# Performance work log

Measured on AMD Instinct MI355X. Metric: run time of the kernel, lower is better.

## Reference

```python
import jax, jax.numpy as jnp
import numpy as np

E = 7          # ensemble_size
STATE = 32
ACTION = 8
HID = [256, 256, 256, 128]
B = 32768


def _init_linear(key, e, fan_in, fan_out):
    kw, kb = jax.random.split(key)
    bound = 1.0 / np.sqrt(fan_in)
    W = jax.random.uniform(kw, (e, fan_in, fan_out), jnp.float32, -bound, bound)
    b = jax.random.uniform(kb, (e, fan_out), jnp.float32, -bound, bound)
    return W, b


def setup_inputs() -> dict:
    key = jax.random.key(0)
    ks = jax.random.split(key, 9)
    state = jax.random.normal(ks[0], (B, STATE), jnp.float32)
    action = jax.random.normal(ks[1], (B, ACTION), jnp.float32)
    dims = [STATE + ACTION] + HID
    W0, b0 = _init_linear(ks[2], E, dims[0], dims[1])
    W1, b1 = _init_linear(ks[3], E, dims[1], dims[2])
    W2, b2 = _init_linear(ks[4], E, dims[2], dims[3])
    W3, b3 = _init_linear(ks[5], E, dims[3], dims[4])
    Wmu, bmu = _init_linear(ks[6], E, dims[4], STATE)
    Wsig, bsig = _init_linear(ks[7], E, dims[4], STATE)
    max_logstd = jnp.ones((STATE,), jnp.float32)
    min_logstd = jnp.full((STATE,), -5.0, jnp.float32)
    return {
        'state': state, 'action': action,
        'W0': W0, 'b0': b0, 'W1': W1, 'b1': b1,
        'W2': W2, 'b2': b2, 'W3': W3, 'b3': b3,
        'Wmu': Wmu, 'bmu': bmu, 'Wsig': Wsig, 'bsig': bsig,
        'max_logstd': max_logstd, 'min_logstd': min_logstd,
    }


def _swish(x):
    return x * jax.nn.sigmoid(x)


def _soft_clamp(x, _min, _max):
    x = _max - jax.nn.softplus(_max - x)
    x = _min + jax.nn.softplus(x - _min)
    return x


def reference(state, action, W0, b0, W1, b1, W2, b2, W3, b3,
              Wmu, bmu, Wsig, bsig, max_logstd, min_logstd):
    # Broadcast inputs to the ensemble axis: [E, B, D]
    x = jnp.concatenate([state, action], axis=-1)            # [B, S+A]
    h = jnp.broadcast_to(x, (E,) + x.shape)                   # [E, B, S+A]
    # Batched per-ensemble GEMM chain (grouped GEMM)
    h = _swish(jnp.einsum('ebi,eio->ebo', h, W0) + b0[:, None, :])
    h = _swish(jnp.einsum('ebi,eio->ebo', h, W1) + b1[:, None, :])
    h = _swish(jnp.einsum('ebi,eio->ebo', h, W2) + b2[:, None, :])
    h = _swish(jnp.einsum('ebi,eio->ebo', h, W3) + b3[:, None, :])
    mu = jnp.einsum('ebi,eio->ebo', h, Wmu) + bmu[:, None, :]         # [E, B, S]
    log_sigma = jnp.einsum('ebi,eio->ebo', h, Wsig) + bsig[:, None, :]
    log_sigma = _soft_clamp(log_sigma, min_logstd, max_logstd)
    sigma = jnp.exp(log_sigma)
    mu = mu + state[None, :, :]                                        # residual
    return mu, sigma
```

## Files before the change

### kernel.cpp

```cpp
#include <hip/hip_runtime.h>
#include <hip/hip_bf16.h>


#define NE 7
#define NB 32768
#define PER_E 188416
#define HSTRIDE 264

typedef __attribute__((ext_vector_type(8))) short short8;
typedef __attribute__((ext_vector_type(4))) float floatx4;

__device__ __forceinline__ short f2b(float f) {
    union { float f; unsigned u; } c; c.f = f;
    return (short)((c.u + 0x7fffu + ((c.u >> 16) & 1u)) >> 16);
}
__device__ __forceinline__ unsigned pk2(float a, float b) {
    union { __hip_bfloat162 h; unsigned u; } c;
    c.h = __float22bfloat162_rn(make_float2(a, b));
    return c.u;
}

__global__ void __launch_bounds__(256) pack_w(
    const float* __restrict__ W0, const float* __restrict__ W1,
    const float* __restrict__ W2, const float* __restrict__ W3,
    const float* __restrict__ Wmu, const float* __restrict__ Wsig,
    short* __restrict__ out)
{
    __shared__ float tile[32][65];
    const int t = threadIdx.x;
    int b = blockIdx.x;
    int e = b / 92;
    int r = b - e * 92;
    const float* src = W0;
    int off = 0, Kact = 40, N = 256, NT = 16, kt, ntb;
    bool inv = false, head = false;
    if (r < 8)       { kt = r >> 2; ntb = r & 3; }
    else if (r < 40) { r -= 8;  src = W1; off = 16384;  Kact = 256; kt = r >> 2; ntb = r & 3; inv = true; }
    else if (r < 72) { r -= 40; src = W2; off = 81920;  Kact = 256; kt = r >> 2; ntb = r & 3; inv = true; }
    else if (r < 88) { r -= 72; src = W3; off = 147456; Kact = 256; N = 128; NT = 8; kt = r >> 1; ntb = r & 1; inv = true; }
    else             { r -= 88; off = 180224; Kact = 128; N = 64; NT = 4; kt = r; ntb = 0; inv = true; head = true; }

#pragma unroll
    for (int i = 0; i < 8; ++i) {
        int elem  = t + i * 256;
        int row_l = elem >> 6, col_l = elem & 63;
        int gk = kt * 32 + row_l;
        int gn = ntb * 64 + col_l;
        float v = 0.f;
        if (gk < Kact) {
            if (head) v = (gn < 32) ? Wmu[((size_t)e * 128 + gk) * 32 + gn]
                                    : Wsig[((size_t)e * 128 + gk) * 32 + (gn - 32)];
            else      v = src[((size_t)e * Kact + gk) * N + gn];
        }
        tile[row_l][col_l] = v;
    }
    __syncthreads();

    const int f = t >> 6, lam = t & 63;
    const int lan = lam & 15, quad = lam >> 4;
    short8 o;
#pragma unroll
    for (int j = 0; j < 8; ++j) {
        int q  = quad * 8 + j;
        int sr = inv ? (((q & 1) << 4) | (q >> 1)) : q;
        o[j] = f2b(tile[sr][f * 16 + lan]);
    }
    *(short8*)(out + (size_t)e * PER_E + off +
               ((size_t)(kt * NT + ntb * 4 + f) * 64 + lam) * 8) = o;
}

template<int KT, int NTW, int NT, int NNTW>
__device__ __forceinline__ void mlp_layer(const short* __restrict__ wpk,
                                          const float* __restrict__ bias,
                                          short* hs, const int wave, const int lane,
                                          const short8* bf0,
                                          const short* __restrict__ nwpk,
                                          short8* nbf0) {
    const int quad = lane >> 4;
    const int lan  = lane & 15;
    floatx4 acc[4][NTW];
#pragma unroll
    for (int mt = 0; mt < 4; ++mt)
#pragma unroll
        for (int nt = 0; nt < NTW; ++nt) acc[mt][nt] = floatx4{0.f, 0.f, 0.f, 0.f};

    short8 bfc[NTW], bfn[NTW];
#pragma unroll
    for (int nt = 0; nt < NTW; ++nt) bfc[nt] = bf0[nt];

#pragma unroll
    for (int kt = 0; kt < KT; ++kt) {
        if (kt + 1 < KT) {
#pragma unroll
            for (int nt = 0; nt < NTW; ++nt)
                bfn[nt] = *(const short8*)(wpk +
                    ((size_t)((kt + 1) * NT + wave * NTW + nt) * 64 + lane) * 8);
        }
        short8 af[4];
#pragma unroll
        for (int mt = 0; mt < 4; ++mt)
            af[mt] = *(const short8*)(hs + (mt * 16 + lan) * HSTRIDE + kt * 32 + quad * 8);
#pragma unroll
        for (int nt = 0; nt < NTW; ++nt)
#pragma unroll
            for (int mt = 0; mt < 4; ++mt)
                acc[mt][nt] = __builtin_amdgcn_mfma_f32_16x16x32_bf16(af[mt], bfc[nt], acc[mt][nt], 0, 0, 0);
#pragma unroll
        for (int nt = 0; nt < NTW; ++nt) bfc[nt] = bfn[nt];
    }

#pragma unroll
    for (int nt = 0; nt < NNTW; ++nt)
        nbf0[nt] = *(const short8*)(nwpk + ((size_t)(wave * NNTW + nt) * 64 + lane) * 8);

    __syncthreads();
#pragma unroll
    for (int np = 0; np < NTW / 2; ++np) {
        const int ntg   = wave * NTW + 2 * np;
        const float bA  = bias[ntg * 16 + lan];
        const float bB  = bias[ntg * 16 + 16 + lan];
        const int pcol  = (ntg >> 1) * 32 + 2 * lan;
#pragma unroll
        for (int mt = 0; mt < 4; ++mt)
#pragma unroll
            for (int r2 = 0; r2 < 4; ++r2) {
                float vA = acc[mt][2 * np][r2] + bA;
                vA = vA * __builtin_amdgcn_rcpf(1.f + __expf(-vA));
                float vB = acc[mt][2 * np + 1][r2] + bB;
                vB = vB * __builtin_amdgcn_rcpf(1.f + __expf(-vB));
                *(unsigned*)(hs + (mt * 16 + quad * 4 + r2) * HSTRIDE + pcol) = pk2(vA, vB);
            }
    }
    __syncthreads();
}

__device__ __forceinline__ float softplus_stable(float x) {
    return fmaxf(x, 0.f) + __logf(1.f + __expf(-fabsf(x)));
}

__global__ void __launch_bounds__(256, 3)
fused_ensemble(const float* __restrict__ state, const float* __restrict__ action,
               const float* __restrict__ b0, const float* __restrict__ b1,
               const float* __restrict__ b2, const float* __restrict__ b3,
               const float* __restrict__ bmu, const float* __restrict__ bsig,
               const float* __restrict__ maxls, const float* __restrict__ minls,
               const short* __restrict__ wpk,
               float* __restrict__ out_mu, float* __restrict__ out_sig) {
    __shared__ __align__(16) short hs[64 * HSTRIDE];
    const int tid  = threadIdx.x;
    const int wave = tid >> 6, lane = tid & 63;
    const int bid  = blockIdx.x;
    const int e    = bid >> 9;
    const int r0   = (bid & 511) << 6;

    const short* wp = wpk + (size_t)e * PER_E;

    short8 fragA[4], fragB[4];
#pragma unroll
    for (int nt = 0; nt < 4; ++nt)
        fragA[nt] = *(const short8*)(wp + ((size_t)(wave * 4 + nt) * 64 + lane) * 8);

    for (int idx = tid; idx < 64 * 32; idx += 256) {
        int m = idx >> 5, cp = idx & 31;
        int row = r0 + m;
        float2 v;
        if (cp < 16)      v = ((const float2*)state)[row * 16 + cp];
        else if (cp < 20) v = ((const float2*)action)[row * 4 + (cp - 16)];
        else              v = make_float2(0.f, 0.f);
        *(unsigned*)(hs + m * HSTRIDE + 2 * cp) = pk2(v.x, v.y);
    }
    __syncthreads();

    mlp_layer<2, 4, 16, 4>(wp,          b0 + e * 256, hs, wave, lane, fragA, wp + 16384,  fragB);
    mlp_layer<8, 4, 16, 4>(wp + 16384,  b1 + e * 256, hs, wave, lane, fragB, wp + 81920,  fragA);
    mlp_layer<8, 4, 16, 2>(wp + 81920,  b2 + e * 256, hs, wave, lane, fragA, wp + 147456, fragB);
    mlp_layer<8, 2, 8, 1 >(wp + 147456, b3 + e * 128, hs, wave, lane, fragB, wp + 180224, fragA);

    const int quad = lane >> 4, lan = lane & 15;
    floatx4 acc[4];
#pragma unroll
    for (int mt = 0; mt < 4; ++mt) acc[mt] = floatx4{0.f, 0.f, 0.f, 0.f};
    const short* wph = wp + 180224;
    short8 bhc = fragA[0], bhn;
#pragma unroll
    for (int kt = 0; kt < 4; ++kt) {
        if (kt < 3)
            bhn = *(const short8*)(wph + (((size_t)(kt + 1) * 4 + wave) * 64 + lane) * 8);
#pragma unroll
        for (int mt = 0; mt < 4; ++mt) {
            const short8 af = *(const short8*)(hs + (mt * 16 + lan) * HSTRIDE + kt * 32 + quad * 8);
            acc[mt] = __builtin_amdgcn_mfma_f32_16x16x32_bf16(af, bhc, acc[mt], 0, 0, 0);
        }
        bhc = bhn;
    }
    const int colw = wave * 16 + lan;
    if (colw < 32) {
        const int col = colw;
        const float bv = bmu[e * 32 + col];
#pragma unroll
        for (int mt = 0; mt < 4; ++mt)
#pragma unroll
            for (int r2 = 0; r2 < 4; ++r2) {
                int grow = r0 + mt * 16 + quad * 4 + r2;
                float v = acc[mt][r2] + bv + state[grow * 32 + col];
                out_mu[((size_t)e * NB + grow) * 32 + col] = v;
            }
    } else {
        const int col = colw - 32;
        const float bv = bsig[e * 32 + col];
        const float mx = maxls[col], mn = minls[col];
#pragma unroll
        for (int mt = 0; mt < 4; ++mt)
#pragma unroll
            for (int r2 = 0; r2 < 4; ++r2) {
                int grow = r0 + mt * 16 + quad * 4 + r2;
                float ls = acc[mt][r2] + bv;
                ls = mx - softplus_stable(mx - ls);
                ls = mn + softplus_stable(ls - mn);
                out_sig[((size_t)e * NB + grow) * 32 + col] = __expf(ls);
            }
    }
}

extern "C" void kernel_launch(void* const* d_in, const int* in_sizes, int n_in,
                              void* d_out, int out_size, void* d_ws, size_t ws_size,
                              hipStream_t stream) {
    const float* state  = (const float*)d_in[0];
    const float* action = (const float*)d_in[1];
    const float* W0   = (const float*)d_in[2];
    const float* b0   = (const float*)d_in[3];
    const float* W1   = (const float*)d_in[4];
    const float* b1   = (const float*)d_in[5];
    const float* W2   = (const float*)d_in[6];
    const float* b2   = (const float*)d_in[7];
    const float* W3   = (const float*)d_in[8];
    const float* b3   = (const float*)d_in[9];
    const float* Wmu  = (const float*)d_in[10];
    const float* bmu  = (const float*)d_in[11];
    const float* Wsig = (const float*)d_in[12];
    const float* bsig = (const float*)d_in[13];
    const float* maxls = (const float*)d_in[14];
    const float* minls = (const float*)d_in[15];

    short* wpk = (short*)d_ws;
    float* out_mu  = (float*)d_out;
    float* out_sig = out_mu + (size_t)NE * NB * 32;

    pack_w<<<NE * 92, 256, 0, stream>>>(W0, W1, W2, W3, Wmu, Wsig, wpk);
    fused_ensemble<<<NE * 512, 256, 0, stream>>>(state, action, b0, b1, b2, b3,
                                                 bmu, bsig, maxls, minls, wpk,
                                                 out_mu, out_sig);
}
```

Before: 227.3 us.

## Overlap each layer's swish epilogue with the next layer's MFMA K-loop

Restructures the MLP chain so the epilogue of one layer (bias, swish, bf16 writeback to LDS) is interleaved with the MFMA accumulation of the next layer. The K-tiles of the next layer are reordered: even K-tiles run first while the second half of the previous epilogue is written, and odd K-tiles run after a barrier. This hides the transcendental/ALU epilogue under matrix-core work, but keeps two accumulator sets live at once, which raises VGPR pressure and may hurt occupancy under the 3-blocks-per-SM launch bound.

```diff
diff --git a/kernel.cpp b/kernel.cpp
--- a/kernel.cpp
+++ b/kernel.cpp
@@ -69,67 +69,90 @@
                ((size_t)(kt * NT + ntb * 4 + f) * 64 + lam) * 8) = o;
 }
 
-template<int KT, int NTW, int NT, int NNTW>
-__device__ __forceinline__ void mlp_layer(const short* __restrict__ wpk,
-                                          const float* __restrict__ bias,
-                                          short* hs, const int wave, const int lane,
-                                          const short8* bf0,
-                                          const short* __restrict__ nwpk,
-                                          short8* nbf0) {
-    const int quad = lane >> 4;
-    const int lan  = lane & 15;
-    floatx4 acc[4][NTW];
-#pragma unroll
-    for (int mt = 0; mt < 4; ++mt)
-#pragma unroll
-        for (int nt = 0; nt < NTW; ++nt) acc[mt][nt] = floatx4{0.f, 0.f, 0.f, 0.f};
-
-    short8 bfc[NTW], bfn[NTW];
-#pragma unroll
-    for (int nt = 0; nt < NTW; ++nt) bfc[nt] = bf0[nt];
-
-#pragma unroll
-    for (int kt = 0; kt < KT; ++kt) {
-        if (kt + 1 < KT) {
-#pragma unroll
-            for (int nt = 0; nt < NTW; ++nt)
-                bfn[nt] = *(const short8*)(wpk +
-                    ((size_t)((kt + 1) * NT + wave * NTW + nt) * 64 + lane) * 8);
-        }
-        short8 af[4];
-#pragma unroll
-        for (int mt = 0; mt < 4; ++mt)
-            af[mt] = *(const short8*)(hs + (mt * 16 + lan) * HSTRIDE + kt * 32 + quad * 8);
-#pragma unroll
-        for (int nt = 0; nt < NTW; ++nt)
-#pragma unroll
-            for (int mt = 0; mt < 4; ++mt)
-                acc[mt][nt] = __builtin_amdgcn_mfma_f32_16x16x32_bf16(af[mt], bfc[nt], acc[mt][nt], 0, 0, 0);
-#pragma unroll
-        for (int nt = 0; nt < NTW; ++nt) bfc[nt] = bfn[nt];
-    }
-
-#pragma unroll
-    for (int nt = 0; nt < NNTW; ++nt)
-        nbf0[nt] = *(const short8*)(nwpk + ((size_t)(wave * NNTW + nt) * 64 + lane) * 8);
-
-    __syncthreads();
-#pragma unroll
-    for (int np = 0; np < NTW / 2; ++np) {
-        const int ntg   = wave * NTW + 2 * np;
-        const float bA  = bias[ntg * 16 + lan];
-        const float bB  = bias[ntg * 16 + 16 + lan];
-        const int pcol  = (ntg >> 1) * 32 + 2 * lan;
-#pragma unroll
-        for (int mt = 0; mt < 4; ++mt)
-#pragma unroll
-            for (int r2 = 0; r2 < 4; ++r2) {
-                float vA = acc[mt][2 * np][r2] + bA;
-                vA = vA * __builtin_amdgcn_rcpf(1.f + __expf(-vA));
-                float vB = acc[mt][2 * np + 1][r2] + bB;
-                vB = vB * __builtin_amdgcn_rcpf(1.f + __expf(-vB));
-                *(unsigned*)(hs + (mt * 16 + quad * 4 + r2) * HSTRIDE + pcol) = pk2(vA, vB);
-            }
+
+template<int NTW, int NT>
+__device__ __forceinline__ void ldb(const short* __restrict__ wpk, int kt,
+                                    int wave, int lane, short8* bf) {
+#pragma unroll
+    for (int nt = 0; nt < NTW; ++nt)
+        bf[nt] = *(const short8*)(wpk + ((size_t)(kt * NT + wave * NTW + nt) * 64 + lane) * 8);
+}
+
+template<int NTW>
+__device__ __forceinline__ void mfma_k(floatx4 (&acc)[4][NTW], const short* hs,
+                                       int kt, int lan, int quad, const short8* bfc) {
+    short8 af[4];
+#pragma unroll
+    for (int mt = 0; mt < 4; ++mt)
+        af[mt] = *(const short8*)(hs + (mt * 16 + lan) * HSTRIDE + kt * 32 + quad * 8);
+#pragma unroll
+    for (int nt = 0; nt < NTW; ++nt)
+#pragma unroll
+        for (int mt = 0; mt < 4; ++mt)
+            acc[mt][nt] = __builtin_amdgcn_mfma_f32_16x16x32_bf16(af[mt], bfc[nt], acc[mt][nt], 0, 0, 0);
+}
+
+__device__ __forceinline__ float swish(float v) {
+    return v * __builtin_amdgcn_rcpf(1.f + __expf(-v));
+}
+
+template<int NTW>
+__device__ __forceinline__ void epi_q(const floatx4 (&acc)[4][NTW], int np, int mt,
+                                      float bA, float bB, short* hs,
+                                      int wave, int lan, int quad) {
+    const int ntg  = wave * NTW + 2 * np;
+    const int pcol = (ntg >> 1) * 32 + 2 * lan;
+#pragma unroll
+    for (int r2 = 0; r2 < 4; ++r2) {
+        float vA = swish(acc[mt][2 * np][r2] + bA);
+        float vB = swish(acc[mt][2 * np + 1][r2] + bB);
+        *(unsigned*)(hs + (mt * 16 + quad * 4 + r2) * HSTRIDE + pcol) = pk2(vA, vB);
+    }
+}
+
+template<int NNTW, int NNT, int XNTW, int XNT>
+__device__ __forceinline__ void layer_step(
+    const short* __restrict__ wpkN, const short* __restrict__ wpkX,
+    const float* __restrict__ biasP,
+    floatx4 (&accP)[4][4], floatx4 (&accN)[4][NNTW],
+    short8 (&bfN)[NNTW], short8 (&bfX)[XNTW],
+    short* hs, int wave, int lane, int lan, int quad)
+{
+    const int ntg0 = wave * 4;
+    const float bA0 = biasP[ntg0 * 16 + lan],       bB0 = biasP[ntg0 * 16 + 16 + lan];
+    const float bA1 = biasP[(ntg0 + 2) * 16 + lan], bB1 = biasP[(ntg0 + 2) * 16 + 16 + lan];
+
+#pragma unroll
+    for (int mt = 0; mt < 4; ++mt)
+        epi_q<4>(accP, 0, mt, bA0, bB0, hs, wave, lan, quad);
+    __syncthreads();
+
+#pragma unroll
+    for (int mt = 0; mt < 4; ++mt)
+#pragma unroll
+        for (int nt = 0; nt < NNTW; ++nt) accN[mt][nt] = floatx4{0.f, 0.f, 0.f, 0.f};
+
+    short8 bfc[NNTW], bfn[NNTW];
+#pragma unroll
+    for (int nt = 0; nt < NNTW; ++nt) bfc[nt] = bfN[nt];
+
+#pragma unroll
+    for (int i = 0; i < 4; ++i) {
+        ldb<NNTW, NNT>(wpkN, (i < 3) ? 2 * i + 2 : 1, wave, lane, bfn);
+        mfma_k<NNTW>(accN, hs, 2 * i, lan, quad, bfc);
+        epi_q<4>(accP, 1, i, bA1, bB1, hs, wave, lan, quad);
+#pragma unroll
+        for (int nt = 0; nt < NNTW; ++nt) bfc[nt] = bfn[nt];
+    }
+    __syncthreads();
+
+#pragma unroll
+    for (int i = 0; i < 4; ++i) {
+        if (i < 3) ldb<NNTW, NNT>(wpkN, 2 * i + 3, wave, lane, bfn);
+        else       ldb<XNTW, XNT>(wpkX, 0, wave, lane, bfX);
+        mfma_k<NNTW>(accN, hs, 2 * i + 1, lan, quad, bfc);
+#pragma unroll
+        for (int nt = 0; nt < NNTW; ++nt) bfc[nt] = bfn[nt];
     }
     __syncthreads();
 }
@@ -149,16 +172,15 @@
     __shared__ __align__(16) short hs[64 * HSTRIDE];
     const int tid  = threadIdx.x;
     const int wave = tid >> 6, lane = tid & 63;
+    const int lan  = lane & 15, quad = lane >> 4;
     const int bid  = blockIdx.x;
     const int e    = bid >> 9;
     const int r0   = (bid & 511) << 6;
 
     const short* wp = wpk + (size_t)e * PER_E;
 
-    short8 fragA[4], fragB[4];
-#pragma unroll
-    for (int nt = 0; nt < 4; ++nt)
-        fragA[nt] = *(const short8*)(wp + ((size_t)(wave * 4 + nt) * 64 + lane) * 8);
+    short8 bfL0[4], bfL0b[4], bfL1[4], bfL2[4], bfL3[2], bfHD[1];
+    ldb<4, 16>(wp, 0, wave, lane, bfL0);
 
     for (int idx = tid; idx < 64 * 32; idx += 256) {
         int m = idx >> 5, cp = idx & 31;
@@ -171,17 +193,40 @@
     }
     __syncthreads();
 
-    mlp_layer<2, 4, 16, 4>(wp,          b0 + e * 256, hs, wave, lane, fragA, wp + 16384,  fragB);
-    mlp_layer<8, 4, 16, 4>(wp + 16384,  b1 + e * 256, hs, wave, lane, fragB, wp + 81920,  fragA);
-    mlp_layer<8, 4, 16, 2>(wp + 81920,  b2 + e * 256, hs, wave, lane, fragA, wp + 147456, fragB);
-    mlp_layer<8, 2, 8, 1 >(wp + 147456, b3 + e * 128, hs, wave, lane, fragB, wp + 180224, fragA);
-
-    const int quad = lane >> 4, lan = lane & 15;
+    floatx4 acc0[4][4], acc1[4][4], acc2[4][4];
+    floatx4 acc3[4][2];
+#pragma unroll
+    for (int mt = 0; mt < 4; ++mt)
+#pragma unroll
+        for (int nt = 0; nt < 4; ++nt) acc0[mt][nt] = floatx4{0.f, 0.f, 0.f, 0.f};
+    ldb<4, 16>(wp, 1, wave, lane, bfL0b);
+    mfma_k<4>(acc0, hs, 0, lan, quad, bfL0);
+    ldb<4, 16>(wp + 16384, 0, wave, lane, bfL1);
+    mfma_k<4>(acc0, hs, 1, lan, quad, bfL0b);
+    __syncthreads();
+
+    layer_step<4, 16, 4, 16>(wp + 16384,  wp + 81920,  b0 + e * 256,
+                             acc0, acc1, bfL1, bfL2, hs, wave, lane, lan, quad);
+    layer_step<4, 16, 2, 8 >(wp + 81920,  wp + 147456, b1 + e * 256,
+                             acc1, acc2, bfL2, bfL3, hs, wave, lane, lan, quad);
+    layer_step<2, 8,  1, 4 >(wp + 147456, wp + 180224, b2 + e * 256,
+                             acc2, acc3, bfL3, bfHD, hs, wave, lane, lan, quad);
+
+    {
+        const int ntg = wave * 2;
+        const float bA = b3[e * 128 + ntg * 16 + lan];
+        const float bB = b3[e * 128 + ntg * 16 + 16 + lan];
+#pragma unroll
+        for (int mt = 0; mt < 4; ++mt)
+            epi_q<2>(acc3, 0, mt, bA, bB, hs, wave, lan, quad);
+    }
+    __syncthreads();
+
     floatx4 acc[4];
 #pragma unroll
     for (int mt = 0; mt < 4; ++mt) acc[mt] = floatx4{0.f, 0.f, 0.f, 0.f};
     const short* wph = wp + 180224;
-    short8 bhc = fragA[0], bhn;
+    short8 bhc = bfHD[0], bhn;
 #pragma unroll
     for (int kt = 0; kt < 4; ++kt) {
         if (kt < 3)
```

Measured after the change: 223.0 us. No clear change (-1.9%).

## Keep activations in registers via transposed MFMA, drop shared-memory staging

Applied to the files above, without the earlier changes.

Swaps the MFMA operands so weights are the A operand and activations the B operand. Each wave then owns 16 batch rows across all output features, and its output accumulator layout matches the next layer's input fragment layout. This removes the LDS activation buffer and the __syncthreads between layers, and the weight packing is permuted to match. In exchange, every wave now loads all weight fragments from global/L2, with no prefetch or cross-wave sharing, which quadruples weight traffic per block. Register pressure also rises because two 8-entry activation arrays and up to 16 accumulators are held per thread.

```diff
diff --git a/kernel.cpp b/kernel.cpp
--- a/kernel.cpp
+++ b/kernel.cpp
@@ -5,10 +5,11 @@
 #define NE 7
 #define NB 32768
 #define PER_E 188416
-#define HSTRIDE 264
 
 typedef __attribute__((ext_vector_type(8))) short short8;
 typedef __attribute__((ext_vector_type(4))) float floatx4;
+
+union S8U { short8 s; unsigned u[4]; };
 
 __device__ __forceinline__ short f2b(float f) {
     union { float f; unsigned u; } c; c.f = f;
@@ -18,6 +19,12 @@
     union { __hip_bfloat162 h; unsigned u; } c;
     c.h = __float22bfloat162_rn(make_float2(a, b));
     return c.u;
+}
+__device__ __forceinline__ float swish(float v) {
+    return v * __builtin_amdgcn_rcpf(1.f + __expf(-v));
+}
+__device__ __forceinline__ float softplus_stable(float x) {
+    return fmaxf(x, 0.f) + __logf(1.f + __expf(-fabsf(x)));
 }
 
 __global__ void __launch_bounds__(256) pack_w(
@@ -26,116 +33,69 @@
     const float* __restrict__ Wmu, const float* __restrict__ Wsig,
     short* __restrict__ out)
 {
-    __shared__ float tile[32][65];
     const int t = threadIdx.x;
-    int b = blockIdx.x;
-    int e = b / 92;
-    int r = b - e * 92;
+    const int b = blockIdx.x;
+    const int e = b / 92;
+    const int r = b - e * 92;
+    const int fid  = r * 4 + (t >> 6);
+    const int lane = t & 63, q = lane >> 4, l = lane & 15;
+
     const float* src = W0;
-    int off = 0, Kact = 40, N = 256, NT = 16, kt, ntb;
-    bool inv = false, head = false;
-    if (r < 8)       { kt = r >> 2; ntb = r & 3; }
-    else if (r < 40) { r -= 8;  src = W1; off = 16384;  Kact = 256; kt = r >> 2; ntb = r & 3; inv = true; }
-    else if (r < 72) { r -= 40; src = W2; off = 81920;  Kact = 256; kt = r >> 2; ntb = r & 3; inv = true; }
-    else if (r < 88) { r -= 72; src = W3; off = 147456; Kact = 256; N = 128; NT = 8; kt = r >> 1; ntb = r & 1; inv = true; }
-    else             { r -= 88; off = 180224; Kact = 128; N = 64; NT = 4; kt = r; ntb = 0; inv = true; head = true; }
-
-#pragma unroll
-    for (int i = 0; i < 8; ++i) {
-        int elem  = t + i * 256;
-        int row_l = elem >> 6, col_l = elem & 63;
-        int gk = kt * 32 + row_l;
-        int gn = ntb * 64 + col_l;
+    int off = 0, Kact = 40, N = 256, NT = 16, kt, mt;
+    bool head = false;
+    if (fid < 32)       { kt = fid >> 4; mt = fid & 15; }
+    else if (fid < 160) { int f = fid - 32;  src = W1; off = 16384;  Kact = 256; kt = f >> 4; mt = f & 15; }
+    else if (fid < 288) { int f = fid - 160; src = W2; off = 81920;  Kact = 256; kt = f >> 4; mt = f & 15; }
+    else if (fid < 352) { int f = fid - 288; src = W3; off = 147456; Kact = 256; N = 128; NT = 8; kt = f >> 3; mt = f & 7; }
+    else                { int f = fid - 352; off = 180224; Kact = 128; N = 64; NT = 4; kt = f >> 2; mt = f & 3; head = true; }
+
+    const int n = head ? (mt * 16 + l)
+                       : ((mt >> 1) * 32 + (l >> 2) * 8 + ((mt & 1) << 2) + (l & 3));
+    short8 o;
+#pragma unroll
+    for (int j = 0; j < 8; ++j) {
+        const int k = kt * 32 + q * 8 + j;
         float v = 0.f;
-        if (gk < Kact) {
-            if (head) v = (gn < 32) ? Wmu[((size_t)e * 128 + gk) * 32 + gn]
-                                    : Wsig[((size_t)e * 128 + gk) * 32 + (gn - 32)];
-            else      v = src[((size_t)e * Kact + gk) * N + gn];
-        }
-        tile[row_l][col_l] = v;
-    }
-    __syncthreads();
-
-    const int f = t >> 6, lam = t & 63;
-    const int lan = lam & 15, quad = lam >> 4;
-    short8 o;
-#pragma unroll
-    for (int j = 0; j < 8; ++j) {
-        int q  = quad * 8 + j;
-        int sr = inv ? (((q & 1) << 4) | (q >> 1)) : q;
-        o[j] = f2b(tile[sr][f * 16 + lan]);
+        if (k < Kact) {
+            if (head) v = (n < 32) ? Wmu[((size_t)e * 128 + k) * 32 + n]
+                                   : Wsig[((size_t)e * 128 + k) * 32 + (n - 32)];
+            else      v = src[((size_t)e * Kact + k) * N + n];
+        }
+        o[j] = f2b(v);
     }
     *(short8*)(out + (size_t)e * PER_E + off +
-               ((size_t)(kt * NT + ntb * 4 + f) * 64 + lam) * 8) = o;
-}
-
-template<int KT, int NTW, int NT, int NNTW>
-__device__ __forceinline__ void mlp_layer(const short* __restrict__ wpk,
+               ((size_t)(kt * NT + mt) * 64 + lane) * 8) = o;
+}
+
+template<int KT, int NT>
+__device__ __forceinline__ void mlp_layer(const short* __restrict__ wfr,
                                           const float* __restrict__ bias,
-                                          short* hs, const int wave, const int lane,
-                                          const short8* bf0,
-                                          const short* __restrict__ nwpk,
-                                          short8* nbf0) {
-    const int quad = lane >> 4;
-    const int lan  = lane & 15;
-    floatx4 acc[4][NTW];
-#pragma unroll
-    for (int mt = 0; mt < 4; ++mt)
-#pragma unroll
-        for (int nt = 0; nt < NTW; ++nt) acc[mt][nt] = floatx4{0.f, 0.f, 0.f, 0.f};
-
-    short8 bfc[NTW], bfn[NTW];
-#pragma unroll
-    for (int nt = 0; nt < NTW; ++nt) bfc[nt] = bf0[nt];
-
+                                          const short8* ain, short8* aout,
+                                          const int lane, const int q) {
+    floatx4 acc[NT];
+#pragma unroll
+    for (int mt = 0; mt < NT; ++mt) acc[mt] = floatx4{0.f, 0.f, 0.f, 0.f};
 #pragma unroll
     for (int kt = 0; kt < KT; ++kt) {
-        if (kt + 1 < KT) {
-#pragma unroll
-            for (int nt = 0; nt < NTW; ++nt)
-                bfn[nt] = *(const short8*)(wpk +
-                    ((size_t)((kt + 1) * NT + wave * NTW + nt) * 64 + lane) * 8);
-        }
-        short8 af[4];
-#pragma unroll
-        for (int mt = 0; mt < 4; ++mt)
-            af[mt] = *(const short8*)(hs + (mt * 16 + lan) * HSTRIDE + kt * 32 + quad * 8);
-#pragma unroll
-        for (int nt = 0; nt < NTW; ++nt)
-#pragma unroll
-            for (int mt = 0; mt < 4; ++mt)
-                acc[mt][nt] = __builtin_amdgcn_mfma_f32_16x16x32_bf16(af[mt], bfc[nt], acc[mt][nt], 0, 0, 0);
-#pragma unroll
-        for (int nt = 0; nt < NTW; ++nt) bfc[nt] = bfn[nt];
-    }
-
-#pragma unroll
-    for (int nt = 0; nt < NNTW; ++nt)
-        nbf0[nt] = *(const short8*)(nwpk + ((size_t)(wave * NNTW + nt) * 64 + lane) * 8);
-
-    __syncthreads();
-#pragma unroll
-    for (int np = 0; np < NTW / 2; ++np) {
-        const int ntg   = wave * NTW + 2 * np;
-        const float bA  = bias[ntg * 16 + lan];
-        const float bB  = bias[ntg * 16 + 16 + lan];
-        const int pcol  = (ntg >> 1) * 32 + 2 * lan;
-#pragma unroll
-        for (int mt = 0; mt < 4; ++mt)
-#pragma unroll
-            for (int r2 = 0; r2 < 4; ++r2) {
-                float vA = acc[mt][2 * np][r2] + bA;
-                vA = vA * __builtin_amdgcn_rcpf(1.f + __expf(-vA));
-                float vB = acc[mt][2 * np + 1][r2] + bB;
-                vB = vB * __builtin_amdgcn_rcpf(1.f + __expf(-vB));
-                *(unsigned*)(hs + (mt * 16 + quad * 4 + r2) * HSTRIDE + pcol) = pk2(vA, vB);
-            }
-    }
-    __syncthreads();
-}
-
-__device__ __forceinline__ float softplus_stable(float x) {
-    return fmaxf(x, 0.f) + __logf(1.f + __expf(-fabsf(x)));
+#pragma unroll
+        for (int mt = 0; mt < NT; ++mt) {
+            const short8 wf = *(const short8*)(wfr +
+                ((size_t)(kt * NT + mt) * 64 + lane) * 8);
+            acc[mt] = __builtin_amdgcn_mfma_f32_16x16x32_bf16(wf, ain[kt], acc[mt], 0, 0, 0);
+        }
+    }
+#pragma unroll
+    for (int kp = 0; kp < NT / 2; ++kp) {
+        const int mA = 2 * kp, mB = 2 * kp + 1;
+        const float4 bA = *(const float4*)(bias + kp * 32 + q * 8);
+        const float4 bB = *(const float4*)(bias + kp * 32 + q * 8 + 4);
+        S8U t;
+        t.u[0] = pk2(swish(acc[mA][0] + bA.x), swish(acc[mA][1] + bA.y));
+        t.u[1] = pk2(swish(acc[mA][2] + bA.z), swish(acc[mA][3] + bA.w));
+        t.u[2] = pk2(swish(acc[mB][0] + bB.x), swish(acc[mB][1] + bB.y));
+        t.u[3] = pk2(swish(acc[mB][2] + bB.z), swish(acc[mB][3] + bB.w));
+        aout[kp] = t.s;
+    }
 }
 
 __global__ void __launch_bounds__(256, 3)
@@ -146,79 +106,97 @@
                const float* __restrict__ maxls, const float* __restrict__ minls,
                const short* __restrict__ wpk,
                float* __restrict__ out_mu, float* __restrict__ out_sig) {
-    __shared__ __align__(16) short hs[64 * HSTRIDE];
     const int tid  = threadIdx.x;
     const int wave = tid >> 6, lane = tid & 63;
+    const int q = lane >> 4, l = lane & 15;
     const int bid  = blockIdx.x;
     const int e    = bid >> 9;
-    const int r0   = (bid & 511) << 6;
+    const int batch = ((bid & 511) << 6) + wave * 16 + l;
 
     const short* wp = wpk + (size_t)e * PER_E;
 
-    short8 fragA[4], fragB[4];
-#pragma unroll
-    for (int nt = 0; nt < 4; ++nt)
-        fragA[nt] = *(const short8*)(wp + ((size_t)(wave * 4 + nt) * 64 + lane) * 8);
-
-    for (int idx = tid; idx < 64 * 32; idx += 256) {
-        int m = idx >> 5, cp = idx & 31;
-        int row = r0 + m;
-        float2 v;
-        if (cp < 16)      v = ((const float2*)state)[row * 16 + cp];
-        else if (cp < 20) v = ((const float2*)action)[row * 4 + (cp - 16)];
-        else              v = make_float2(0.f, 0.f);
-        *(unsigned*)(hs + m * HSTRIDE + 2 * cp) = pk2(v.x, v.y);
-    }
-    __syncthreads();
-
-    mlp_layer<2, 4, 16, 4>(wp,          b0 + e * 256, hs, wave, lane, fragA, wp + 16384,  fragB);
-    mlp_layer<8, 4, 16, 4>(wp + 16384,  b1 + e * 256, hs, wave, lane, fragB, wp + 81920,  fragA);
-    mlp_layer<8, 4, 16, 2>(wp + 81920,  b2 + e * 256, hs, wave, lane, fragA, wp + 147456, fragB);
-    mlp_layer<8, 2, 8, 1 >(wp + 147456, b3 + e * 128, hs, wave, lane, fragB, wp + 180224, fragA);
-
-    const int quad = lane >> 4, lan = lane & 15;
+    short8 actA[8], actB[8];
+
+    {
+        const float4* sp = (const float4*)(state + (size_t)batch * 32 + q * 8);
+        const float4 s0 = sp[0], s1 = sp[1];
+        S8U t;
+        t.u[0] = pk2(s0.x, s0.y); t.u[1] = pk2(s0.z, s0.w);
+        t.u[2] = pk2(s1.x, s1.y); t.u[3] = pk2(s1.z, s1.w);
+        actB[0] = t.s;
+        if (q == 0) {
+            const float4* ap = (const float4*)(action + (size_t)batch * 8);
+            const float4 a0 = ap[0], a1 = ap[1];
+            S8U u;
+            u.u[0] = pk2(a0.x, a0.y); u.u[1] = pk2(a0.z, a0.w);
+            u.u[2] = pk2(a1.x, a1.y); u.u[3] = pk2(a1.z, a1.w);
+            actB[1] = u.s;
+        } else {
+            actB[1] = short8{0, 0, 0, 0, 0, 0, 0, 0};
+        }
+    }
+
+    mlp_layer<2, 16>(wp,           b0 + e * 256, actB, actA, lane, q);
+    mlp_layer<8, 16>(wp + 16384,   b1 + e * 256, actA, actB, lane, q);
+    mlp_layer<8, 16>(wp + 81920,   b2 + e * 256, actB, actA, lane, q);
+    mlp_layer<8, 8 >(wp + 147456,  b3 + e * 128, actA, actB, lane, q);
+
     floatx4 acc[4];
 #pragma unroll
     for (int mt = 0; mt < 4; ++mt) acc[mt] = floatx4{0.f, 0.f, 0.f, 0.f};
     const short* wph = wp + 180224;
-    short8 bhc = fragA[0], bhn;
 #pragma unroll
     for (int kt = 0; kt < 4; ++kt) {
-        if (kt < 3)
-            bhn = *(const short8*)(wph + (((size_t)(kt + 1) * 4 + wave) * 64 + lane) * 8);
 #pragma unroll
         for (int mt = 0; mt < 4; ++mt) {
-            const short8 af = *(const short8*)(hs + (mt * 16 + lan) * HSTRIDE + kt * 32 + quad * 8);
-            acc[mt] = __builtin_amdgcn_mfma_f32_16x16x32_bf16(af, bhc, acc[mt], 0, 0, 0);
-        }
-        bhc = bhn;
-    }
-    const int colw = wave * 16 + lan;
-    if (colw < 32) {
-        const int col = colw;
-        const float bv = bmu[e * 32 + col];
-#pragma unroll
-        for (int mt = 0; mt < 4; ++mt)
-#pragma unroll
-            for (int r2 = 0; r2 < 4; ++r2) {
-                int grow = r0 + mt * 16 + quad * 4 + r2;
-                float v = acc[mt][r2] + bv + state[grow * 32 + col];
-                out_mu[((size_t)e * NB + grow) * 32 + col] = v;
-            }
-    } else {
-        const int col = colw - 32;
-        const float bv = bsig[e * 32 + col];
-        const float mx = maxls[col], mn = minls[col];
-#pragma unroll
-        for (int mt = 0; mt < 4; ++mt)
-#pragma unroll
-            for (int r2 = 0; r2 < 4; ++r2) {
-                int grow = r0 + mt * 16 + quad * 4 + r2;
-                float ls = acc[mt][r2] + bv;
-                ls = mx - softplus_stable(mx - ls);
-                ls = mn + softplus_stable(ls - mn);
-                out_sig[((size_t)e * NB + grow) * 32 + col] = __expf(ls);
-            }
+            const short8 wf = *(const short8*)(wph + ((size_t)(kt * 4 + mt) * 64 + lane) * 8);
+            acc[mt] = __builtin_amdgcn_mfma_f32_16x16x32_bf16(wf, actB[kt], acc[mt], 0, 0, 0);
+        }
+    }
+#pragma unroll
+    for (int mt = 0; mt < 2; ++mt) {
+        const int c0 = mt * 16 + q * 4;
+        const float4 bv = *(const float4*)(bmu + e * 32 + c0);
+        const float4 st = *(const float4*)(state + (size_t)batch * 32 + c0);
+        float4 o;
+        o.x = acc[mt][0] + bv.x + st.x;
+        o.y = acc[mt][1] + bv.y + st.y;
+        o.z = acc[mt][2] + bv.z + st.z;
+        o.w = acc[mt][3] + bv.w + st.w;
+        *(float4*)(out_mu + ((size_t)e * NB + batch) * 32 + c0) = o;
+    }
+#pragma unroll
+    for (int mt = 2; mt < 4; ++mt) {
+        const int c0 = (mt - 2) * 16 + q * 4;
+        const float4 bv = *(const float4*)(bsig + e * 32 + c0);
+        const float4 mx = *(const float4*)(maxls + c0);
+        const float4 mn = *(const float4*)(minls + c0);
+        float4 o;
+        {
+            float ls = acc[mt][0] + bv.x;
+            ls = mx.x - softplus_stable(mx.x - ls);
+            ls = mn.x + softplus_stable(ls - mn.x);
+            o.x = __expf(ls);
+        }
+        {
+            float ls = acc[mt][1] + bv.y;
+            ls = mx.y - softplus_stable(mx.y - ls);
+            ls = mn.y + softplus_stable(ls - mn.y);
+            o.y = __expf(ls);
+        }
+        {
+            float ls = acc[mt][2] + bv.z;
+            ls = mx.z - softplus_stable(mx.z - ls);
+            ls = mn.z + softplus_stable(ls - mn.z);
+            o.z = __expf(ls);
+        }
+        {
+            float ls = acc[mt][3] + bv.w;
+            ls = mx.w - softplus_stable(mx.w - ls);
+            ls = mn.w + softplus_stable(ls - mn.w);
+            o.w = __expf(ls);
+        }
+        *(float4*)(out_sig + ((size_t)e * NB + batch) * 32 + c0) = o;
     }
 }
 
```

Measured after the change: 460.6 us. 2.03x slower.
